# Optimization experiments

Measured on AMD Instinct MI355X. Metric: run time of the kernel, lower is better.

Reference implementation:

```python
import jax, jax.numpy as jnp
import numpy as np


def setup_inputs() -> dict:
    key = jax.random.key(0)
    Y = jax.random.normal(key, (16384, 2048), dtype=jnp.float32)
    return {"Y": Y}


def reference(Y):
    # Original: Y = Y / sqrt(n); D = Y.T @ Y; loss = sum(sqrt((1 - diag(D))**2))
    # diag(Y.T @ Y) == per-column sum of squares -> O(n*d) instead of O(n*d^2)
    n = Y.shape[0]
    Yn = Y / jnp.sqrt(jnp.asarray(n, dtype=Y.dtype))
    diag = jnp.sum(Yn * Yn, axis=0)  # [d]
    loss = jnp.sum(jnp.abs(1.0 - diag))  # sqrt(x**2) == |x|
    return loss
```

## Files before the change

kernel.cpp:

```cpp
#include <hip/hip_runtime.h>

#define NROWS 16384
#define D     2048
#define D4    (D / 4)
#define YBLOCKS 256
#define ROWS_PER_BLOCK (NROWS / YBLOCKS)

__global__ void __launch_bounds__(256)
colsq_partial(const float4* __restrict__ Y4, float4* __restrict__ P4) {
    const int c4 = blockIdx.x * 256 + threadIdx.x;
    const int yb = blockIdx.y;
    const float4* p = Y4 + (size_t)yb * ROWS_PER_BLOCK * D4 + c4;
    float4 acc = make_float4(0.f, 0.f, 0.f, 0.f);
#pragma unroll 8
    for (int r = 0; r < ROWS_PER_BLOCK; ++r) {
        float4 v = p[(size_t)r * D4];
        acc.x += v.x * v.x;
        acc.y += v.y * v.y;
        acc.z += v.z * v.z;
        acc.w += v.w * v.w;
    }
    P4[(size_t)yb * D4 + c4] = acc;
}

__global__ void __launch_bounds__(256)
finalize(const float* __restrict__ P, float* __restrict__ out) {
    const int c = blockIdx.x * 256 + threadIdx.x;
    float s = 0.f;
#pragma unroll 8
    for (int yb = 0; yb < YBLOCKS; ++yb)
        s += P[yb * D + c];
    float v = fabsf(1.0f - s * (1.0f / (float)NROWS));
#pragma unroll
    for (int off = 32; off; off >>= 1)
        v += __shfl_down(v, off, 64);
    __shared__ float lds[4];
    const int lane = threadIdx.x & 63;
    const int wv   = threadIdx.x >> 6;
    if (lane == 0) lds[wv] = v;
    __syncthreads();
    if (threadIdx.x == 0) {
        float b = lds[0] + lds[1] + lds[2] + lds[3];
        atomicAdd(out, b);
    }
}

extern "C" void kernel_launch(void* const* d_in, const int* in_sizes, int n_in,
                              void* d_out, int out_size, void* d_ws, size_t ws_size,
                              hipStream_t stream) {
    const float4* Y4 = (const float4*)d_in[0];
    float* out = (float*)d_out;
    float* P   = (float*)d_ws;

    hipMemsetAsync(out, 0, sizeof(float), stream);

    colsq_partial<<<dim3(2, YBLOCKS), 256, 0, stream>>>(Y4, (float4*)d_ws);
    finalize<<<dim3(8), 256, 0, stream>>>(P, out);
}
```

Before: 202.0 us.

## Fuse column partials and finalize into one kernel via atomics and last-block reduction

```diff
diff --git a/kernel.cpp b/kernel.cpp
--- a/kernel.cpp
+++ b/kernel.cpp
@@ -5,14 +5,16 @@
 #define D4    (D / 4)
 #define YBLOCKS 256
 #define ROWS_PER_BLOCK (NROWS / YBLOCKS)
+#define NBLOCKS (2 * YBLOCKS)
 
 __global__ void __launch_bounds__(256)
-colsq_partial(const float4* __restrict__ Y4, float4* __restrict__ P4) {
+semidef_loss(const float4* __restrict__ Y4, float* __restrict__ colsum,
+             unsigned* __restrict__ counter, float* __restrict__ out) {
     const int c4 = blockIdx.x * 256 + threadIdx.x;
     const int yb = blockIdx.y;
     const float4* p = Y4 + (size_t)yb * ROWS_PER_BLOCK * D4 + c4;
     float4 acc = make_float4(0.f, 0.f, 0.f, 0.f);
-#pragma unroll 8
+#pragma unroll 16
     for (int r = 0; r < ROWS_PER_BLOCK; ++r) {
         float4 v = p[(size_t)r * D4];
         acc.x += v.x * v.x;
@@ -20,40 +22,51 @@
         acc.z += v.z * v.z;
         acc.w += v.w * v.w;
     }
-    P4[(size_t)yb * D4 + c4] = acc;
-}
+    const int c = c4 * 4;
+    atomicAdd(&colsum[c + 0], acc.x);
+    atomicAdd(&colsum[c + 1], acc.y);
+    atomicAdd(&colsum[c + 2], acc.z);
+    atomicAdd(&colsum[c + 3], acc.w);
 
-__global__ void __launch_bounds__(256)
-finalize(const float* __restrict__ P, float* __restrict__ out) {
-    const int c = blockIdx.x * 256 + threadIdx.x;
-    float s = 0.f;
-#pragma unroll 8
-    for (int yb = 0; yb < YBLOCKS; ++yb)
-        s += P[yb * D + c];
-    float v = fabsf(1.0f - s * (1.0f / (float)NROWS));
+    __threadfence();
+    __shared__ int is_last;
+    if (threadIdx.x == 0) {
+        unsigned old = __hip_atomic_fetch_add(counter, 1u, __ATOMIC_ACQ_REL,
+                                              __HIP_MEMORY_SCOPE_AGENT);
+        is_last = (old == NBLOCKS - 1);
+    }
+    __syncthreads();
+    if (!is_last) return;
+
+    float vsum = 0.f;
+#pragma unroll
+    for (int i = 0; i < 8; ++i) {
+        int col = threadIdx.x + 256 * i;
+        float s = __hip_atomic_load(&colsum[col], __ATOMIC_RELAXED,
+                                    __HIP_MEMORY_SCOPE_AGENT);
+        vsum += fabsf(1.0f - s * (1.0f / (float)NROWS));
+    }
 #pragma unroll
     for (int off = 32; off; off >>= 1)
-        v += __shfl_down(v, off, 64);
+        vsum += __shfl_down(vsum, off, 64);
     __shared__ float lds[4];
     const int lane = threadIdx.x & 63;
     const int wv   = threadIdx.x >> 6;
-    if (lane == 0) lds[wv] = v;
+    if (lane == 0) lds[wv] = vsum;
     __syncthreads();
-    if (threadIdx.x == 0) {
-        float b = lds[0] + lds[1] + lds[2] + lds[3];
-        atomicAdd(out, b);
-    }
+    if (threadIdx.x == 0)
+        out[0] = lds[0] + lds[1] + lds[2] + lds[3];
 }
 
 extern "C" void kernel_launch(void* const* d_in, const int* in_sizes, int n_in,
                               void* d_out, int out_size, void* d_ws, size_t ws_size,
                               hipStream_t stream) {
     const float4* Y4 = (const float4*)d_in[0];
-    float* out = (float*)d_out;
-    float* P   = (float*)d_ws;
+    float* out       = (float*)d_out;
+    float* colsum    = (float*)d_ws;
+    unsigned* counter = (unsigned*)((char*)d_ws + D * sizeof(float));
 
-    hipMemsetAsync(out, 0, sizeof(float), stream);
+    hipMemsetAsync(d_ws, 0, D * sizeof(float) + sizeof(unsigned), stream);
 
-    colsq_partial<<<dim3(2, YBLOCKS), 256, 0, stream>>>(Y4, (float4*)d_ws);
-    finalize<<<dim3(8), 256, 0, stream>>>(P, out);
+    semidef_loss<<<dim3(2, YBLOCKS), 256, 0, stream>>>(Y4, colsum, counter, out);
 }
```

Measured after the change: 276.5 us. 1.37x slower.

## Double row-split blocks and parallelize finalize across more blocks without atomics

Applied to the files above, without the earlier changes.

```diff
diff --git a/kernel.cpp b/kernel.cpp
--- a/kernel.cpp
+++ b/kernel.cpp
@@ -3,7 +3,7 @@
 #define NROWS 16384
 #define D     2048
 #define D4    (D / 4)
-#define YBLOCKS 256
+#define YBLOCKS 512
 #define ROWS_PER_BLOCK (NROWS / YBLOCKS)
 
 __global__ void __launch_bounds__(256)
@@ -24,25 +24,36 @@
 }
 
 __global__ void __launch_bounds__(256)
-finalize(const float* __restrict__ P, float* __restrict__ out) {
-    const int c = blockIdx.x * 256 + threadIdx.x;
+col_finalize(const float* __restrict__ P, float* __restrict__ ws2) {
+    const int col  = blockIdx.x * 64 + (threadIdx.x & 63);
+    const int part = threadIdx.x >> 6;
     float s = 0.f;
 #pragma unroll 8
-    for (int yb = 0; yb < YBLOCKS; ++yb)
-        s += P[yb * D + c];
-    float v = fabsf(1.0f - s * (1.0f / (float)NROWS));
+    for (int i = 0; i < YBLOCKS / 4; ++i) {
+        int yb = part * (YBLOCKS / 4) + i;
+        s += P[yb * D + col];
+    }
+    __shared__ float lds[256];
+    lds[threadIdx.x] = s;
+    __syncthreads();
+    if (threadIdx.x < 64) {
+        float tot = lds[threadIdx.x] + lds[threadIdx.x + 64] +
+                    lds[threadIdx.x + 128] + lds[threadIdx.x + 192];
+        float v = fabsf(1.0f - tot * (1.0f / (float)NROWS));
+#pragma unroll
+        for (int off = 32; off; off >>= 1)
+            v += __shfl_down(v, off, 64);
+        if (threadIdx.x == 0) ws2[blockIdx.x] = v;
+    }
+}
+
+__global__ void __launch_bounds__(64)
+final_sum(const float* __restrict__ ws2, float* __restrict__ out) {
+    float v = (threadIdx.x < 32) ? ws2[threadIdx.x] : 0.f;
 #pragma unroll
     for (int off = 32; off; off >>= 1)
         v += __shfl_down(v, off, 64);
-    __shared__ float lds[4];
-    const int lane = threadIdx.x & 63;
-    const int wv   = threadIdx.x >> 6;
-    if (lane == 0) lds[wv] = v;
-    __syncthreads();
-    if (threadIdx.x == 0) {
-        float b = lds[0] + lds[1] + lds[2] + lds[3];
-        atomicAdd(out, b);
-    }
+    if (threadIdx.x == 0) out[0] = v;
 }
 
 extern "C" void kernel_launch(void* const* d_in, const int* in_sizes, int n_in,
@@ -51,9 +62,9 @@
     const float4* Y4 = (const float4*)d_in[0];
     float* out = (float*)d_out;
     float* P   = (float*)d_ws;
+    float* ws2 = (float*)((char*)d_ws + (size_t)YBLOCKS * D * sizeof(float));
 
-    hipMemsetAsync(out, 0, sizeof(float), stream);
-
-    colsq_partial<<<dim3(2, YBLOCKS), 256, 0, stream>>>(Y4, (float4*)d_ws);
-    finalize<<<dim3(8), 256, 0, stream>>>(P, out);
+    colsq_partial<<<dim3(2, YBLOCKS), 256, 0, stream>>>(Y4, (float4*)P);
+    col_finalize<<<dim3(32), 256, 0, stream>>>(P, ws2);
+    final_sum<<<dim3(1), 64, 0, stream>>>(ws2, out);
 }
```

After: 194.7 us. 3.6% less time.
